# Kernel optimization log

Hardware: AMD Instinct MI355X
Metric: run time of the kernel (lower is better)

Reference implementation:

```python
import jax, jax.numpy as jnp
import numpy as np

PIXEL_SIZE = 0.1
PI = 3.141592653589793


def setup_inputs() -> dict:
    key = jax.random.key(0)
    batch = jax.random.normal(key, (128, 1, 512, 512), dtype=jnp.float32)
    return {"batch": batch}


def _hann_window(roi):
    # lin = linspace(-roi/2, roi/2, roi); r[i,j] = sqrt(lin[j]^2 + lin[i]^2)
    lin = jnp.linspace(-roi / 2, roi / 2, roi, dtype=jnp.float32)
    r = jnp.sqrt(lin[None, :] ** 2 + lin[:, None] ** 2)
    hann = 0.5 * (1.0 + jnp.cos(PI * r / (roi / 2)))
    hann = jnp.where(r > roi / 2, 0.0, hann)
    return hann  # [roi, roi]


def _radial_segments(roi, n_freq):
    # radialDst = round(sqrt(xx^2 + yy^2)) with x = arange(-cx, roi-cx)
    cx = roi // 2
    x = np.arange(-cx, roi - cx, dtype=np.float64)
    xx, yy = np.meshgrid(x, x, indexing="ij")
    rad = np.round(np.sqrt(xx ** 2 + yy ** 2)).astype(np.int32)
    # bins >= n_freq go into an overflow segment that is discarded
    seg = np.where(rad < n_freq, rad, n_freq)
    return jnp.asarray(seg.ravel())


def reference(batch):
    px = PIXEL_SIZE
    roi = batch.shape[-1]
    cx = roi // 2
    n_freq = cx + 1
    nyquist = 1.0 / (2.0 * px)

    # subtract per-ROI mean
    batch_nm = batch - jnp.mean(batch, axis=(2, 3), keepdims=True)

    # Hann-windowed 2D power spectrum, averaged over realizations
    hann = _hann_window(roi)[None, None, :, :]
    F = jnp.fft.fftshift(jnp.fft.fft2(batch_nm * hann, axes=(2, 3)), axes=(2, 3))
    ps = jnp.mean(jnp.abs(F) ** 2, axis=0)            # [1, roi, roi]
    nps2D = (px ** 2 / roi ** 2) * jnp.squeeze(ps)    # [roi, roi]

    # single-pass radial mean binning (replaces per-k boolean-mask loop)
    seg = _radial_segments(roi, n_freq)
    flat = nps2D.ravel()
    sums = jax.ops.segment_sum(flat, seg, num_segments=n_freq + 1)[:n_freq]
    counts = jax.ops.segment_sum(jnp.ones_like(flat), seg, num_segments=n_freq + 1)[:n_freq]
    nps1D = sums / counts

    f1D = jnp.linspace(0.0, nyquist, n_freq, dtype=jnp.float32)
    return nps1D, nps2D, f1D
```

## Files before the change

### kernel.cpp

```cpp
#include <hip/hip_runtime.h>
#include <hip/hip_fp16.h>

#define N 512
#define NF 257
#define NB 128
#define PI_F 3.14159265358979323846f
#define C_SQ2 0.70710678118654752440f

typedef float f2 __attribute__((ext_vector_type(2)));
__device__ __forceinline__ f2 F2(float x, float y) { f2 r; r.x = x; r.y = y; return r; }

__device__ __forceinline__ f2 cmul(f2 a, f2 b) {
    return a.xx * b + F2(-a.y, a.y) * b.yx;
}
__device__ __forceinline__ void bf(f2& a, f2& b) {
    f2 t = b;
    b = a - t;
    a = a + t;
}
__device__ __forceinline__ void bf_tw(f2& a, f2& b, f2 w) {
    f2 t = cmul(b, w);
    b = a - t;
    a = a + t;
}
__device__ __forceinline__ void bf_ni(f2& a, f2& b) {
    f2 t = F2(b.y, -b.x);
    b = a - t;
    a = a + t;
}
__device__ __forceinline__ void lds_order() {
    asm volatile("" ::: "memory");
}
__device__ __forceinline__ f2 bperm(int pa, f2 v) {
    int xi = __builtin_amdgcn_ds_bpermute(pa, __float_as_int(v.x));
    int yi = __builtin_amdgcn_ds_bpermute(pa, __float_as_int(v.y));
    return F2(__int_as_float(xi), __int_as_float(yi));
}

__device__ __forceinline__ void fft_phaseA(f2 v[8]) {
    const f2 w64  = F2(C_SQ2, -C_SQ2);
    const f2 w192 = F2(-C_SQ2, -C_SQ2);
    bf(v[0], v[1]); bf(v[2], v[3]); bf(v[4], v[5]); bf(v[6], v[7]);
    bf(v[0], v[2]); bf_ni(v[1], v[3]); bf(v[4], v[6]); bf_ni(v[5], v[7]);
    bf(v[0], v[4]); bf_tw(v[1], v[5], w64); bf_ni(v[2], v[6]); bf_tw(v[3], v[7], w192);
}
__device__ __forceinline__ void fft_phaseBC(f2 v[8], f2 W1, f2 W1a,
                                            f2 W1n, f2 W1c, f2 W2,
                                            f2 W2n, f2 W3) {
    bf_tw(v[0], v[1], W3); bf_tw(v[2], v[3], W3); bf_tw(v[4], v[5], W3); bf_tw(v[6], v[7], W3);
    bf_tw(v[0], v[2], W2); bf_tw(v[1], v[3], W2n); bf_tw(v[4], v[6], W2); bf_tw(v[5], v[7], W2n);
    bf_tw(v[0], v[4], W1); bf_tw(v[1], v[5], W1a); bf_tw(v[2], v[6], W1n); bf_tw(v[3], v[7], W1c);
}

__device__ __forceinline__ void fft512_core(f2 v[8], f2* st, int l) {
    const f2 w64  = F2(C_SQ2, -C_SQ2);
    const f2 w192 = F2(-C_SQ2, -C_SQ2);
    int g = l >> 3, r = l & 7;
    lds_order();
    fft_phaseA(v);
#pragma unroll
    for (int e = 0; e < 8; e++) st[9 * l + e] = v[e];
    lds_order();
#pragma unroll
    for (int t = 0; t < 8; t++) v[t] = st[72 * g + 9 * t + r];
    float sn, cs;
    __sincosf(-(PI_F / 32.0f) * (float)r, &sn, &cs);
    f2 W1 = F2(cs, sn);
    f2 W2 = cmul(W1, W1);
    f2 W3 = cmul(W2, W2);
    f2 W2n = F2(W2.y, -W2.x);
    f2 W1a = cmul(W1, w64);
    f2 W1n = F2(W1.y, -W1.x);
    f2 W1c = cmul(W1, w192);
    fft_phaseBC(v, W1, W1a, W1n, W1c, W2, W2n, W3);
    lds_order();
#pragma unroll
    for (int t = 0; t < 8; t++) st[72 * g + 9 * t + r] = v[t];
    lds_order();
#pragma unroll
    for (int t = 0; t < 8; t++) v[t] = st[72 * t + l + (l >> 3)];
    __sincosf(-(PI_F / 256.0f) * (float)l, &sn, &cs);
    f2 Wc = F2(cs, sn);
    f2 w2 = cmul(Wc, Wc);
    f2 w4 = cmul(w2, w2);
    f2 w2n = F2(w2.y, -w2.x);
    f2 Wca = cmul(Wc, w64);
    f2 Wcn = F2(Wc.y, -Wc.x);
    f2 Wcc = cmul(Wc, w192);
    fft_phaseBC(v, Wc, Wca, Wcn, Wcc, w2, w2n, w4);
}

__device__ __forceinline__ void fft512_x2(f2 va[8], f2 vb[8], f2* st, int l) {
    const f2 w64  = F2(C_SQ2, -C_SQ2);
    const f2 w192 = F2(-C_SQ2, -C_SQ2);
    int g = l >> 3, r = l & 7;
    fft_phaseA(va); fft_phaseA(vb);
    lds_order();
#pragma unroll
    for (int e = 0; e < 8; e++) st[9 * l + e] = va[e];
    lds_order();
#pragma unroll
    for (int t = 0; t < 8; t++) va[t] = st[72 * g + 9 * t + r];
    lds_order();
#pragma unroll
    for (int e = 0; e < 8; e++) st[9 * l + e] = vb[e];
    lds_order();
#pragma unroll
    for (int t = 0; t < 8; t++) vb[t] = st[72 * g + 9 * t + r];
    float sn, cs;
    __sincosf(-(PI_F / 32.0f) * (float)r, &sn, &cs);
    f2 W1 = F2(cs, sn);
    f2 W2 = cmul(W1, W1);
    f2 W3 = cmul(W2, W2);
    f2 W2n = F2(W2.y, -W2.x);
    f2 W1a = cmul(W1, w64);
    f2 W1n = F2(W1.y, -W1.x);
    f2 W1c = cmul(W1, w192);
    fft_phaseBC(va, W1, W1a, W1n, W1c, W2, W2n, W3);
    fft_phaseBC(vb, W1, W1a, W1n, W1c, W2, W2n, W3);
    lds_order();
#pragma unroll
    for (int t = 0; t < 8; t++) st[72 * g + 9 * t + r] = va[t];
    lds_order();
#pragma unroll
    for (int t = 0; t < 8; t++) va[t] = st[72 * t + l + (l >> 3)];
    lds_order();
#pragma unroll
    for (int t = 0; t < 8; t++) st[72 * g + 9 * t + r] = vb[t];
    lds_order();
#pragma unroll
    for (int t = 0; t < 8; t++) vb[t] = st[72 * t + l + (l >> 3)];
    __sincosf(-(PI_F / 256.0f) * (float)l, &sn, &cs);
    f2 Wc = F2(cs, sn);
    f2 w2 = cmul(Wc, Wc);
    f2 w4 = cmul(w2, w2);
    f2 w2n = F2(w2.y, -w2.x);
    f2 Wca = cmul(Wc, w64);
    f2 Wcn = F2(Wc.y, -Wc.x);
    f2 Wcc = cmul(Wc, w192);
    fft_phaseBC(va, Wc, Wca, Wcn, Wcc, w2, w2n, w4);
    fft_phaseBC(vb, Wc, Wca, Wcn, Wcc, w2, w2n, w4);
}

__device__ __forceinline__ void unpack_rows(const f2 v[8], __half2* tile,
                                            int lr0, int lr1, int l, int sl) {
#pragma unroll
    for (int t = 0; t <= 4; t++) {
        f2 a = v[7 - t];
        float zfx = __shfl(a.x, sl);
        float zfy = __shfl(a.y, sl);
        if (l == 0) { f2 o = v[(8 - t) & 7]; zfx = o.x; zfy = o.y; }
        f2 z = v[t];
        int col = 64 * t + l;
        if (col < NF) {
            tile[lr0 * 265 + col] = __floats2half2_rn(0.5f * (z.x + zfx), 0.5f * (z.y - zfy));
            tile[lr1 * 265 + col] = __floats2half2_rn(0.5f * (z.y + zfy), 0.5f * (zfx - z.x));
        }
    }
}

__global__ __launch_bounds__(256) void hanntab_zero_kernel(float* __restrict__ htab,
                                                           float* __restrict__ accH,
                                                           float* __restrict__ bins,
                                                           float* __restrict__ meanacc) {
    int i = blockIdx.x * 256 + threadIdx.x;
    int r = i >> 9, c = i & (N - 1);
    const float step = (float)N / (float)(N - 1);
    float a = -0.5f * (float)N + (float)r * step;
    float b = -0.5f * (float)N + (float)c * step;
    float rr = sqrtf(a * a + b * b);
    float h = (rr > 256.0f) ? 0.0f : 0.5f * (1.0f + cosf(rr * (PI_F / 256.0f)));
    htab[i] = h;
    if (i < NF * N) accH[i] = 0.0f;
    if (i < 2 * (NF + 1)) bins[i] = 0.0f;
    if (i < NB) meanacc[i] = 0.0f;
}

__global__ __launch_bounds__(512) void hannfft_kernel(const float* __restrict__ htab,
                                                      f2* __restrict__ Hrow) {
    __shared__ __align__(16) float sm[9216];
    int tid = threadIdx.x;
    int w = tid >> 6, l = tid & 63;
    int rowbase = blockIdx.x << 4;
    int r1 = rowbase + 2 * w;
    int pa = (__brev((unsigned)l) >> 26) << 2;
    int sl = (64 - l) & 63;
    const int bre[8] = {0, 4, 2, 6, 1, 5, 3, 7};
    const float* h1 = htab + (size_t)r1 * N + l;
    const float* h2 = h1 + N;

    f2 v[8];
#pragma unroll
    for (int e = 0; e < 8; e++) {
        int o = bre[e] << 6;
        v[e] = F2(h1[o], h2[o]);
    }
#pragma unroll
    for (int e = 0; e < 8; e++) v[e] = bperm(pa, v[e]);

    f2* st = (f2*)sm + w * 576;
    fft512_core(v, st, l);
    __syncthreads();

    float* tre = sm;
    float* tim = sm + 4240;
    int lr0 = 2 * w, lr1 = lr0 + 1;
#pragma unroll
    for (int t = 0; t <= 4; t++) {
        f2 a = v[7 - t];
        float zfx = __shfl(a.x, sl);
        float zfy = __shfl(a.y, sl);
        if (l == 0) { f2 o = v[(8 - t) & 7]; zfx = o.x; zfy = o.y; }
        f2 z = v[t];
        int col = 64 * t + l;
        if (col < NF) {
            tre[lr0 * 265 + col] = 0.5f * (z.x + zfx);
            tim[lr0 * 265 + col] = 0.5f * (z.y - zfy);
            tre[lr1 * 265 + col] = 0.5f * (z.y + zfy);
            tim[lr1 * 265 + col] = 0.5f * (zfx - z.x);
        }
    }
    __syncthreads();

    int c0 = tid >> 4, rr = tid & 15;
#pragma unroll
    for (int it = 0; it < 9; it++) {
        int c = it * 32 + c0;
        if (c < NF) {
            Hrow[(size_t)c * N + rowbase + rr] = F2(tre[rr * 265 + c], tim[rr * 265 + c]);
        }
    }
}

__global__ __launch_bounds__(512, 6) void rowfft_kernel(const float* __restrict__ x,
                                                        const float* __restrict__ htab,
                                                        float* __restrict__ meanacc,
                                                        __half2* __restrict__ inter) {
    __shared__ __align__(16) float sm[9216];
    __shared__ float redsum[8];
    int tid = threadIdx.x;
    int w = tid >> 6, l = tid & 63;
    int img = blockIdx.x >> 4;
    int rowbase = (blockIdx.x & 15) << 5;
    int r1 = rowbase + 4 * w;
    int pa = (__brev((unsigned)l) >> 26) << 2;
    int sl = (64 - l) & 63;
    const int bre[8] = {0, 4, 2, 6, 1, 5, 3, 7};
    const float* xp = x + ((size_t)img * N + r1) * N + l;
    const float* hp = htab + (size_t)r1 * N + l;

    float ax[4][8], hx[4][8];
#pragma unroll
    for (int j = 0; j < 4; j++)
#pragma unroll
        for (int e = 0; e < 8; e++) ax[j][e] = xp[j * N + (bre[e] << 6)];
#pragma unroll
    for (int j = 0; j < 4; j++)
#pragma unroll
        for (int e = 0; e < 8; e++) hx[j][e] = hp[j * N + (bre[e] << 6)];
    __builtin_amdgcn_sched_barrier(0);

    float rsum = 0.0f;
#pragma unroll
    for (int j = 0; j < 4; j++)
#pragma unroll
        for (int e = 0; e < 8; e++) rsum += ax[j][e];

    f2 va[8], vb[8];
#pragma unroll
    for (int e = 0; e < 8; e++) {
        va[e] = bperm(pa, F2(ax[0][e] * hx[0][e], ax[1][e] * hx[1][e]));
        vb[e] = bperm(pa, F2(ax[2][e] * hx[2][e], ax[3][e] * hx[3][e]));
    }

#pragma unroll
    for (int off = 32; off > 0; off >>= 1) rsum += __shfl_down(rsum, off);
    if (l == 0) redsum[w] = rsum;

    f2* st = (f2*)sm + w * 576;
    fft512_x2(va, vb, st, l);
    __syncthreads();
    if (tid == 0) {
        float s = 0.0f;
#pragma unroll
        for (int i = 0; i < 8; i++) s += redsum[i];
        atomicAdd(meanacc + img, s);
    }

    __half2* tile = (__half2*)sm;
    unpack_rows(va, tile, 4 * w, 4 * w + 1, l, sl);
    unpack_rows(vb, tile, 4 * w + 2, 4 * w + 3, l, sl);
    __syncthreads();

    int c0 = tid >> 5, rr = tid & 31;
#pragma unroll
    for (int it = 0; it < 17; it++) {
        int c = it * 16 + c0;
        if (c < NF) {
            inter[((size_t)img * NF + c) * N + rowbase + rr] = tile[rr * 265 + c];
        }
    }
}

__global__ __launch_bounds__(256, 4) void colfft_kernel(const __half2* __restrict__ inter,
                                                        const f2* __restrict__ Hrow,
                                                        const float* __restrict__ meanacc,
                                                        float* __restrict__ accH) {
    __shared__ __align__(16) float sm[4608];
    int tid = threadIdx.x;
    int w = tid >> 6, l = tid & 63;
    int col = blockIdx.x * 4 + w;
    int colc = col < NF ? col : NF - 1;
    int b0 = blockIdx.y * 4;
    f2* st = (f2*)sm + w * 576;
    int pa = (__brev((unsigned)l) >> 26) << 2;
    const int bre[8] = {0, 4, 2, 6, 1, 5, 3, 7};

    f2 hc[8];
    const f2* hp = Hrow + (size_t)colc * N + l;
#pragma unroll
    for (int e = 0; e < 8; e++) hc[e] = hp[bre[e] << 6];

    float mn[4];
#pragma unroll
    for (int i = 0; i < 4; i++)
        mn[i] = meanacc[b0 + i] * (1.0f / ((float)N * (float)N));

    float pw[8];
#pragma unroll
    for (int t = 0; t < 8; t++) pw[t] = 0.0f;

    const size_t istr = (size_t)NF * N;
    const __half2* base = inter + ((size_t)b0 * NF + colc) * N + l;

    __half2 cA[8], cB[8], nA[8], nB[8];
#pragma unroll
    for (int e = 0; e < 8; e++) {
        cA[e] = base[bre[e] << 6];
        cB[e] = base[istr + (bre[e] << 6)];
    }
    __builtin_amdgcn_sched_barrier(0);

#pragma unroll
    for (int it = 0; it < 2; it++) {
        if (it == 0) {
#pragma unroll
            for (int e = 0; e < 8; e++) {
                nA[e] = base[2 * istr + (bre[e] << 6)];
                nB[e] = base[3 * istr + (bre[e] << 6)];
            }
        }
        float mA = mn[2 * it], mB = mn[2 * it + 1];
        f2 va[8], vb[8];
#pragma unroll
        for (int e = 0; e < 8; e++) {
            float2 zA = __half22float2(cA[e]);
            float2 zB = __half22float2(cB[e]);
            va[e] = bperm(pa, F2(zA.x, zA.y) - mA * hc[e]);
            vb[e] = bperm(pa, F2(zB.x, zB.y) - mB * hc[e]);
        }
        fft512_x2(va, vb, st, l);
#pragma unroll
        for (int t = 0; t < 8; t++)
            pw[t] += va[t].x * va[t].x + va[t].y * va[t].y
                   + vb[t].x * vb[t].x + vb[t].y * vb[t].y;
#pragma unroll
        for (int e = 0; e < 8; e++) { cA[e] = nA[e]; cB[e] = nB[e]; }
    }

    if (col < NF) {
#pragma unroll
        for (int t = 0; t < 8; t++)
            atomicAdd(&accH[(size_t)col * N + 64 * t + l], pw[t]);
    }
}

__global__ __launch_bounds__(256) void finalize2d_kernel(const float* __restrict__ accH,
                                                         float* __restrict__ out2d,
                                                         float* __restrict__ bins) {
    __shared__ float lsum[NF];
    __shared__ float lcnt[NF];
    int t = threadIdx.x;
    for (int i = t; i < NF; i += 256) { lsum[i] = 0.0f; lcnt[i] = 0.0f; }
    __syncthreads();
    const float scale = (0.1f * 0.1f) / ((float)N * (float)N) / (float)NB;
    int idx = blockIdx.x * 256 + t;
    int stride = gridDim.x * 256;
    for (int p = idx; p < N * N; p += stride) {
        int i = p >> 9, j = p & (N - 1);
        int jm = (j + 256) & 511;
        int col, k;
        if (jm < NF) { col = jm; k = (i + 256) & 511; }
        else         { col = 256 - j; k = (256 - i) & 511; }
        float v = accH[((size_t)col << 9) + k] * scale;
        out2d[p] = v;
        float xi = (float)(i - 256), yj = (float)(j - 256);
        int rad = (int)rintf(sqrtf(xi * xi + yj * yj));
        if (rad < NF) { atomicAdd(&lsum[rad], v); atomicAdd(&lcnt[rad], 1.0f); }
    }
    __syncthreads();
    for (int i = t; i < NF; i += 256) {
        if (lsum[i] != 0.0f || lcnt[i] != 0.0f) {
            atomicAdd(&bins[i], lsum[i]);
            atomicAdd(&bins[NF + 1 + i], lcnt[i]);
        }
    }
}

__global__ void finalize1d_kernel(const float* __restrict__ bins, float* __restrict__ out) {
    int t = blockIdx.x * blockDim.x + threadIdx.x;
    if (t < NF) {
        out[t] = bins[t] / bins[NF + 1 + t];
        out[NF + N * N + t] = (float)t * (5.0f / 256.0f);
    }
}

extern "C" void kernel_launch(void* const* d_in, const int* in_sizes, int n_in,
                              void* d_out, int out_size, void* d_ws, size_t ws_size,
                              hipStream_t stream) {
    const float* x = (const float*)d_in[0];
    float* out = (float*)d_out;
    char* ws = (char*)d_ws;

    float* accH    = (float*)ws;
    float* meanacc = (float*)(ws + (size_t)NF * N * sizeof(float));
    float* bins    = meanacc + NB;
    size_t off_h = (size_t)NF * N * sizeof(float) + NB * sizeof(float)
                   + 2 * (NF + 1) * sizeof(float);
    off_h = (off_h + 255) & ~(size_t)255;
    f2* Hrow = (f2*)(ws + off_h);
    size_t off_t = off_h + (size_t)NF * N * sizeof(f2);
    off_t = (off_t + 255) & ~(size_t)255;
    float* htab = (float*)(ws + off_t);
    size_t off_inter = off_t + (size_t)N * N * sizeof(float);
    off_inter = (off_inter + 255) & ~(size_t)255;
    __half2* inter = (__half2*)(ws + off_inter);

    hanntab_zero_kernel<<<dim3(N * N / 256), dim3(256), 0, stream>>>(htab, accH, bins, meanacc);
    hannfft_kernel<<<dim3(32), dim3(512), 0, stream>>>(htab, Hrow);
    rowfft_kernel<<<dim3(NB * 16), dim3(512), 0, stream>>>(x, htab, meanacc, inter);
    colfft_kernel<<<dim3(65, 32), dim3(256), 0, stream>>>(inter, Hrow, meanacc, accH);
    finalize2d_kernel<<<dim3(512), dim3(256), 0, stream>>>(accH, out + NF, bins);
    finalize1d_kernel<<<dim3(2), dim3(256), 0, stream>>>(bins, out);
}
```

Before: 256.6 us.

## Write row FFT output directly from registers as packed 16-byte stores

The row FFT kernel no longer stages its unpacked half-precision output in shared memory for a transpose. Each wave unpacks its four rows in registers using lane shuffles and writes 16-byte vectors holding four rows per column straight to the intermediate buffer. The per-block mean reduction through shared memory and its barriers is replaced with one atomic add per wave, and the launch-bounds occupancy hint drops from 6 to 4. This removes two block barriers and the shared-memory round trip. In exchange each store covers only 16 bytes per column, making it more scattered, and there are eight times as many atomics.

```diff
diff --git a/kernel.cpp b/kernel.cpp
--- a/kernel.cpp
+++ b/kernel.cpp
@@ -232,12 +232,11 @@
     }
 }
 
-__global__ __launch_bounds__(512, 6) void rowfft_kernel(const float* __restrict__ x,
+__global__ __launch_bounds__(512, 4) void rowfft_kernel(const float* __restrict__ x,
                                                         const float* __restrict__ htab,
                                                         float* __restrict__ meanacc,
                                                         __half2* __restrict__ inter) {
     __shared__ __align__(16) float sm[9216];
-    __shared__ float redsum[8];
     int tid = threadIdx.x;
     int w = tid >> 6, l = tid & 63;
     int img = blockIdx.x >> 4;
@@ -275,30 +274,33 @@
 
 #pragma unroll
     for (int off = 32; off > 0; off >>= 1) rsum += __shfl_down(rsum, off);
-    if (l == 0) redsum[w] = rsum;
+    if (l == 0) atomicAdd(meanacc + img, rsum);
 
     f2* st = (f2*)sm + w * 576;
     fft512_x2(va, vb, st, l);
-    __syncthreads();
-    if (tid == 0) {
-        float s = 0.0f;
-#pragma unroll
-        for (int i = 0; i < 8; i++) s += redsum[i];
-        atomicAdd(meanacc + img, s);
-    }
-
-    __half2* tile = (__half2*)sm;
-    unpack_rows(va, tile, 4 * w, 4 * w + 1, l, sl);
-    unpack_rows(vb, tile, 4 * w + 2, 4 * w + 3, l, sl);
-    __syncthreads();
-
-    int c0 = tid >> 5, rr = tid & 31;
-#pragma unroll
-    for (int it = 0; it < 17; it++) {
-        int c = it * 16 + c0;
-        if (c < NF) {
-            inter[((size_t)img * NF + c) * N + rowbase + rr] = tile[rr * 265 + c];
-        }
+
+    union PK { uint4 u; __half2 h[4]; } pk;
+    uint4* ip = (uint4*)inter;
+    size_t cstr = 128;
+    size_t ibase = ((size_t)img * NF) * cstr + (rowbase >> 2) + w;
+#pragma unroll
+    for (int t = 0; t <= 4; t++) {
+        f2 a = va[7 - t];
+        float zfax = __shfl(a.x, sl);
+        float zfay = __shfl(a.y, sl);
+        if (l == 0) { f2 o = va[(8 - t) & 7]; zfax = o.x; zfay = o.y; }
+        f2 z = va[t];
+        pk.h[0] = __floats2half2_rn(0.5f * (z.x + zfax), 0.5f * (z.y - zfay));
+        pk.h[1] = __floats2half2_rn(0.5f * (z.y + zfay), 0.5f * (zfax - z.x));
+        f2 b = vb[7 - t];
+        float zfbx = __shfl(b.x, sl);
+        float zfby = __shfl(b.y, sl);
+        if (l == 0) { f2 o = vb[(8 - t) & 7]; zfbx = o.x; zfby = o.y; }
+        f2 zb = vb[t];
+        pk.h[2] = __floats2half2_rn(0.5f * (zb.x + zfbx), 0.5f * (zb.y - zfby));
+        pk.h[3] = __floats2half2_rn(0.5f * (zb.y + zfby), 0.5f * (zfbx - zb.x));
+        int col = 64 * t + l;
+        if (col < NF) ip[ibase + (size_t)col * cstr] = pk.u;
     }
 }
 
```

Result: slower. 312.7 us (+21.9%).
